# Kernel tuning notes

Measured on AMD Instinct MI355X. Metric: run time of the kernel, lower is better.

The kernel has to match this reference:

```python
import jax, jax.numpy as jnp
import numpy as np
from jax import lax

B, S, FEAT, OUT = 64, 8192, 8, 64


def setup_inputs() -> dict:
    key = jax.random.key(0)
    ks = jax.random.split(key, 7)
    x = jax.random.normal(ks[0], (B, S, FEAT), dtype=jnp.float32)
    # torch default init: U(-1/sqrt(fan_in), 1/sqrt(fan_in))
    def uinit(k, shape, fan_in):
        bound = 1.0 / np.sqrt(fan_in)
        return jax.random.uniform(k, shape, jnp.float32, -bound, bound)
    W1 = uinit(ks[1], (32, 1, 2, 2), 1 * 2 * 2)   # OIHW
    b1 = uinit(ks[2], (32,), 1 * 2 * 2)
    W2 = uinit(ks[3], (32, 32, 1, 2), 32 * 1 * 2)
    b2 = uinit(ks[4], (32,), 32 * 1 * 2)
    Wp = uinit(ks[5], (OUT, 64), 64)              # torch Linear: [out, in]
    bp = uinit(ks[6], (OUT,), 64)
    return {"x": x, "W1": W1, "b1": b1, "W2": W2, "b2": b2, "Wp": Wp, "bp": bp}


def reference(x, W1, b1, W2, b2, Wp, bp):
    b, s, _ = x.shape
    xg = x.reshape(b * s, 1, 2, 4)  # [N,1,2,4] NCHW
    dn = ("NCHW", "OIHW", "NCHW")
    h = lax.conv_general_dilated(xg, W1, (1, 1), "VALID", dimension_numbers=dn)
    h = jax.nn.relu(h + b1[None, :, None, None])          # [N,32,1,3]
    h = lax.conv_general_dilated(h, W2, (1, 1), "VALID", dimension_numbers=dn)
    h = jax.nn.relu(h + b2[None, :, None, None])          # [N,32,1,2]
    h = h.reshape(b * s, 64)                              # C*H*W flatten, matches torch
    out = h @ Wp.T + bp                                   # [N,64]
    return out.reshape(b, s, -1)
```

## Files before the change

kernel.cpp:

```cpp
#include <hip/hip_runtime.h>

typedef __attribute__((ext_vector_type(8))) __bf16 bf16x8;
typedef __attribute__((ext_vector_type(8))) ushort ushort8;
typedef __attribute__((ext_vector_type(4))) float floatx4;

union FragU { ushort8 u; bf16x8 b; };

__device__ inline ushort bf1(float a){
  unsigned u = __float_as_uint(a);
  return (ushort)((u + 0x7FFFu + ((u >> 16) & 1u)) >> 16);
}
__device__ inline unsigned bfpack(float lo, float hi){
  return (unsigned)bf1(lo) | ((unsigned)bf1(hi) << 16);
}

#define BLOCKS 1024

__global__ __launch_bounds__(256) void cnn_fused(
    const float* __restrict__ x,  const float* __restrict__ W1,
    const float* __restrict__ b1, const float* __restrict__ W2,
    const float* __restrict__ b2, const float* __restrict__ Wp,
    const float* __restrict__ bp, float* __restrict__ out, int niter)
{
  __shared__ __align__(16) ushort h2buf[4 * 16 * 72];
  const int tid  = threadIdx.x;
  const int wid  = tid >> 6;
  const int lane = tid & 63;
  const int lm   = lane & 15;
  const int quad = lane >> 4;
  ushort*   myh2 = &h2buf[wid * (16 * 72)];
  unsigned* h2d  = (unsigned*)myh2;

  FragU w2f[2][2];
  #pragma unroll
  for (int t = 0; t < 2; ++t)
    #pragma unroll
    for (int h = 0; h < 2; ++h)
      #pragma unroll
      for (int j = 0; j < 8; ++j)
        w2f[t][h].u[j] = bf1(W2[(t*16 + lm)*64 + (quad*8 + j)*2 + h]);

  FragU wpf[4][2];
  #pragma unroll
  for (int t = 0; t < 4; ++t)
    #pragma unroll
    for (int h = 0; h < 2; ++h)
      #pragma unroll
      for (int j = 0; j < 8; ++j){
        const int c   = h*32 + quad*8 + j;
        const int cp  = c & 31;
        const int oc2 = (cp >> 1) | ((cp & 1) << 4);
        wpf[t][h].u[j] = bf1(Wp[(4*lm + t)*64 + oc2*2 + h]);
      }

  float w1r[8][4], b1r[8];
  #pragma unroll
  for (int i = 0; i < 8; ++i){
    const int oc = quad*8 + i;
    w1r[i][0] = W1[oc*4+0]; w1r[i][1] = W1[oc*4+1];
    w1r[i][2] = W1[oc*4+2]; w1r[i][3] = W1[oc*4+3];
    b1r[i]    = b1[oc];
  }
  const float  b2a = b2[lm], b2b = b2[16 + lm];
  const float4 bp4 = ((const float4*)bp)[lm];

  const long gw   = (long)blockIdx.x * 4 + wid;
  long tilebase   = gw * ((long)niter * 16);

  const float4* x4 = (const float4*)x;
  float4 xa = x4[2*(tilebase + lm)];
  float4 xb = x4[2*(tilebase + lm) + 1];

  const floatx4 z = {0.f, 0.f, 0.f, 0.f};

  for (int it = 0; it < niter; ++it){
    float4 nxa, nxb;
    if (it + 1 < niter){
      const long nr = tilebase + 16 + lm;
      nxa = x4[2*nr]; nxb = x4[2*nr + 1];
    }

    FragU F0, F1, F2;
    #pragma unroll
    for (int i = 0; i < 8; ++i){
      const float w00 = w1r[i][0], w01 = w1r[i][1];
      const float w10 = w1r[i][2], w11 = w1r[i][3], bb = b1r[i];
      F0.u[i] = bf1(fmaxf(0.f, bb + w00*xa.x + w01*xa.y + w10*xb.x + w11*xb.y));
      F1.u[i] = bf1(fmaxf(0.f, bb + w00*xa.y + w01*xa.z + w10*xb.y + w11*xb.z));
      F2.u[i] = bf1(fmaxf(0.f, bb + w00*xa.z + w01*xa.w + w10*xb.z + w11*xb.w));
    }

    floatx4 a00 = z, a01 = z, a10 = z, a11 = z;
    a00 = __builtin_amdgcn_mfma_f32_16x16x32_bf16(F0.b, w2f[0][0].b, a00, 0,0,0);
    a00 = __builtin_amdgcn_mfma_f32_16x16x32_bf16(F1.b, w2f[0][1].b, a00, 0,0,0);
    a01 = __builtin_amdgcn_mfma_f32_16x16x32_bf16(F0.b, w2f[1][0].b, a01, 0,0,0);
    a01 = __builtin_amdgcn_mfma_f32_16x16x32_bf16(F1.b, w2f[1][1].b, a01, 0,0,0);
    a10 = __builtin_amdgcn_mfma_f32_16x16x32_bf16(F1.b, w2f[0][0].b, a10, 0,0,0);
    a10 = __builtin_amdgcn_mfma_f32_16x16x32_bf16(F2.b, w2f[0][1].b, a10, 0,0,0);
    a11 = __builtin_amdgcn_mfma_f32_16x16x32_bf16(F1.b, w2f[1][0].b, a11, 0,0,0);
    a11 = __builtin_amdgcn_mfma_f32_16x16x32_bf16(F2.b, w2f[1][1].b, a11, 0,0,0);

    #pragma unroll
    for (int rg = 0; rg < 4; ++rg){
      const int rr = (quad*4 + rg) * 36;
      h2d[rr +      lm] = bfpack(fmaxf(0.f, a00[rg] + b2a), fmaxf(0.f, a01[rg] + b2b));
      h2d[rr + 16 + lm] = bfpack(fmaxf(0.f, a10[rg] + b2a), fmaxf(0.f, a11[rg] + b2b));
    }
    __syncthreads();

    FragU ca0, ca1;
    ca0.u = *(const ushort8*)&myh2[lm*72 +      quad*8];
    ca1.u = *(const ushort8*)&myh2[lm*72 + 32 + quad*8];

    floatx4 oacc[4];
    #pragma unroll
    for (int t = 0; t < 4; ++t){
      floatx4 acc = z;
      acc = __builtin_amdgcn_mfma_f32_16x16x32_bf16(ca0.b, wpf[t][0].b, acc, 0,0,0);
      acc = __builtin_amdgcn_mfma_f32_16x16x32_bf16(ca1.b, wpf[t][1].b, acc, 0,0,0);
      oacc[t] = acc;
    }

    #pragma unroll
    for (int rg = 0; rg < 4; ++rg){
      float4 v;
      v.x = oacc[0][rg] + bp4.x;
      v.y = oacc[1][rg] + bp4.y;
      v.z = oacc[2][rg] + bp4.z;
      v.w = oacc[3][rg] + bp4.w;
      *(float4*)(out + (tilebase + quad*4 + rg)*64 + 4*lm) = v;
    }
    __syncthreads();

    if (it + 1 < niter){ xa = nxa; xb = nxb; tilebase += 16; }
  }
}

extern "C" void kernel_launch(void* const* d_in, const int* in_sizes, int n_in,
                              void* d_out, int out_size, void* d_ws, size_t ws_size,
                              hipStream_t stream)
{
  const float* x  = (const float*)d_in[0];
  const float* W1 = (const float*)d_in[1];
  const float* b1 = (const float*)d_in[2];
  const float* W2 = (const float*)d_in[3];
  const float* b2 = (const float*)d_in[4];
  const float* Wp = (const float*)d_in[5];
  const float* bp = (const float*)d_in[6];
  float* out = (float*)d_out;

  const int rows  = in_sizes[0] / 8;
  const int tiles = rows / 16;
  const int niter = tiles / (BLOCKS * 4);
  cnn_fused<<<BLOCKS, 256, 0, stream>>>(x, W1, b1, W2, b2, Wp, bp, out, niter);
}
```

Baseline: 180.2 us.

## Keep conv2 output in registers by transposing MFMA operands, drop LDS round-trip

Swaps the A/B operands of the conv2 MFMAs so the accumulator layout directly matches the B-fragment layout the projection MFMA needs. The intermediate no longer goes through shared memory, and both per-iteration __syncthreads barriers are removed. The Wp fragment permutation and the b2 bias indexing are rearranged to match. It also switches bf16 rounding to the compiler's native conversion and doubles the block count, which halves per-wave iterations.

```diff
diff --git a/kernel.cpp b/kernel.cpp
--- a/kernel.cpp
+++ b/kernel.cpp
@@ -6,15 +6,12 @@
 
 union FragU { ushort8 u; bf16x8 b; };
 
-__device__ inline ushort bf1(float a){
-  unsigned u = __float_as_uint(a);
-  return (ushort)((u + 0x7FFFu + ((u >> 16) & 1u)) >> 16);
-}
-__device__ inline unsigned bfpack(float lo, float hi){
-  return (unsigned)bf1(lo) | ((unsigned)bf1(hi) << 16);
+__device__ inline ushort bfu(float a){
+  __bf16 h = (__bf16)a;
+  return __builtin_bit_cast(ushort, h);
 }
 
-#define BLOCKS 1024
+#define BLOCKS 2048
 
 __global__ __launch_bounds__(256) void cnn_fused(
     const float* __restrict__ x,  const float* __restrict__ W1,
@@ -22,14 +19,11 @@
     const float* __restrict__ b2, const float* __restrict__ Wp,
     const float* __restrict__ bp, float* __restrict__ out, int niter)
 {
-  __shared__ __align__(16) ushort h2buf[4 * 16 * 72];
   const int tid  = threadIdx.x;
   const int wid  = tid >> 6;
   const int lane = tid & 63;
   const int lm   = lane & 15;
   const int quad = lane >> 4;
-  ushort*   myh2 = &h2buf[wid * (16 * 72)];
-  unsigned* h2d  = (unsigned*)myh2;
 
   FragU w2f[2][2];
   #pragma unroll
@@ -38,7 +32,7 @@
     for (int h = 0; h < 2; ++h)
       #pragma unroll
       for (int j = 0; j < 8; ++j)
-        w2f[t][h].u[j] = bf1(W2[(t*16 + lm)*64 + (quad*8 + j)*2 + h]);
+        w2f[t][h].u[j] = bfu(W2[(t*16 + lm)*64 + (quad*8 + j)*2 + h]);
 
   FragU wpf[4][2];
   #pragma unroll
@@ -47,10 +41,9 @@
     for (int h = 0; h < 2; ++h)
       #pragma unroll
       for (int j = 0; j < 8; ++j){
-        const int c   = h*32 + quad*8 + j;
-        const int cp  = c & 31;
+        const int cp  = quad*8 + j;
         const int oc2 = (cp >> 1) | ((cp & 1) << 4);
-        wpf[t][h].u[j] = bf1(Wp[(4*lm + t)*64 + oc2*2 + h]);
+        wpf[t][h].u[j] = bfu(Wp[(4*lm + t)*64 + oc2*2 + h]);
       }
 
   float w1r[8][4], b1r[8];
@@ -61,7 +54,12 @@
     w1r[i][2] = W1[oc*4+2]; w1r[i][3] = W1[oc*4+3];
     b1r[i]    = b1[oc];
   }
-  const float  b2a = b2[lm], b2b = b2[16 + lm];
+  float b2lo[4], b2hi[4];
+  #pragma unroll
+  for (int rg = 0; rg < 4; ++rg){
+    b2lo[rg] = b2[     quad*4 + rg];
+    b2hi[rg] = b2[16 + quad*4 + rg];
+  }
   const float4 bp4 = ((const float4*)bp)[lm];
 
   const long gw   = (long)blockIdx.x * 4 + wid;
@@ -85,32 +83,29 @@
     for (int i = 0; i < 8; ++i){
       const float w00 = w1r[i][0], w01 = w1r[i][1];
       const float w10 = w1r[i][2], w11 = w1r[i][3], bb = b1r[i];
-      F0.u[i] = bf1(fmaxf(0.f, bb + w00*xa.x + w01*xa.y + w10*xb.x + w11*xb.y));
-      F1.u[i] = bf1(fmaxf(0.f, bb + w00*xa.y + w01*xa.z + w10*xb.y + w11*xb.z));
-      F2.u[i] = bf1(fmaxf(0.f, bb + w00*xa.z + w01*xa.w + w10*xb.z + w11*xb.w));
+      F0.u[i] = bfu(fmaxf(0.f, bb + w00*xa.x + w01*xa.y + w10*xb.x + w11*xb.y));
+      F1.u[i] = bfu(fmaxf(0.f, bb + w00*xa.y + w01*xa.z + w10*xb.y + w11*xb.z));
+      F2.u[i] = bfu(fmaxf(0.f, bb + w00*xa.z + w01*xa.w + w10*xb.z + w11*xb.w));
     }
 
     floatx4 a00 = z, a01 = z, a10 = z, a11 = z;
-    a00 = __builtin_amdgcn_mfma_f32_16x16x32_bf16(F0.b, w2f[0][0].b, a00, 0,0,0);
-    a00 = __builtin_amdgcn_mfma_f32_16x16x32_bf16(F1.b, w2f[0][1].b, a00, 0,0,0);
-    a01 = __builtin_amdgcn_mfma_f32_16x16x32_bf16(F0.b, w2f[1][0].b, a01, 0,0,0);
-    a01 = __builtin_amdgcn_mfma_f32_16x16x32_bf16(F1.b, w2f[1][1].b, a01, 0,0,0);
-    a10 = __builtin_amdgcn_mfma_f32_16x16x32_bf16(F1.b, w2f[0][0].b, a10, 0,0,0);
-    a10 = __builtin_amdgcn_mfma_f32_16x16x32_bf16(F2.b, w2f[0][1].b, a10, 0,0,0);
-    a11 = __builtin_amdgcn_mfma_f32_16x16x32_bf16(F1.b, w2f[1][0].b, a11, 0,0,0);
-    a11 = __builtin_amdgcn_mfma_f32_16x16x32_bf16(F2.b, w2f[1][1].b, a11, 0,0,0);
+    a00 = __builtin_amdgcn_mfma_f32_16x16x32_bf16(w2f[0][0].b, F0.b, a00, 0,0,0);
+    a00 = __builtin_amdgcn_mfma_f32_16x16x32_bf16(w2f[0][1].b, F1.b, a00, 0,0,0);
+    a01 = __builtin_amdgcn_mfma_f32_16x16x32_bf16(w2f[1][0].b, F0.b, a01, 0,0,0);
+    a01 = __builtin_amdgcn_mfma_f32_16x16x32_bf16(w2f[1][1].b, F1.b, a01, 0,0,0);
+    a10 = __builtin_amdgcn_mfma_f32_16x16x32_bf16(w2f[0][0].b, F1.b, a10, 0,0,0);
+    a10 = __builtin_amdgcn_mfma_f32_16x16x32_bf16(w2f[0][1].b, F2.b, a10, 0,0,0);
+    a11 = __builtin_amdgcn_mfma_f32_16x16x32_bf16(w2f[1][0].b, F1.b, a11, 0,0,0);
+    a11 = __builtin_amdgcn_mfma_f32_16x16x32_bf16(w2f[1][1].b, F2.b, a11, 0,0,0);
 
+    FragU ca0, ca1;
     #pragma unroll
     for (int rg = 0; rg < 4; ++rg){
-      const int rr = (quad*4 + rg) * 36;
-      h2d[rr +      lm] = bfpack(fmaxf(0.f, a00[rg] + b2a), fmaxf(0.f, a01[rg] + b2b));
-      h2d[rr + 16 + lm] = bfpack(fmaxf(0.f, a10[rg] + b2a), fmaxf(0.f, a11[rg] + b2b));
+      ca0.u[2*rg  ] = bfu(fmaxf(0.f, a00[rg] + b2lo[rg]));
+      ca0.u[2*rg+1] = bfu(fmaxf(0.f, a01[rg] + b2hi[rg]));
+      ca1.u[2*rg  ] = bfu(fmaxf(0.f, a10[rg] + b2lo[rg]));
+      ca1.u[2*rg+1] = bfu(fmaxf(0.f, a11[rg] + b2hi[rg]));
     }
-    __syncthreads();
-
-    FragU ca0, ca1;
-    ca0.u = *(const ushort8*)&myh2[lm*72 +      quad*8];
-    ca1.u = *(const ushort8*)&myh2[lm*72 + 32 + quad*8];
 
     floatx4 oacc[4];
     #pragma unroll
@@ -130,7 +125,6 @@
       v.w = oacc[3][rg] + bp4.w;
       *(float4*)(out + (tilebase + quad*4 + rg)*64 + 4*lm) = v;
     }
-    __syncthreads();
 
     if (it + 1 < niter){ xa = nxa; xb = nxb; tilebase += 16; }
   }
```

Measured after the change: 184.2 us. +2.2%, slower.
